# Kernel tuning notes

Hardware: AMD Instinct MI355X
Metric: run time of the kernel (lower is better)

Reference implementation:

```python
import jax, jax.numpy as jnp
import numpy as np

N = 150000
K = 64
C = 128


def setup_inputs() -> dict:
    key = jax.random.key(0)
    k1, k2, k3, k4 = jax.random.split(key, 4)
    H = 512
    W = 512
    pX = jax.random.randint(k1, (N,), 0, W, dtype=jnp.int32)
    pY = jax.random.randint(k2, (N,), 0, H, dtype=jnp.int32)
    vertMask = jax.random.normal(k3, (K, N), dtype=jnp.float32)
    feature = jax.random.normal(k4, (C, K), dtype=jnp.float32)
    return {"H": H, "W": W, "pX": pX, "pY": pY, "vertMask": vertMask, "feature": feature}


def reference(H, W, pX, pY, vertMask, feature):
    # [C, K] @ [K, N] -> [C, N]
    vals = jnp.matmul(feature, vertMask)
    out = jnp.zeros((feature.shape[0], H, W), dtype=feature.dtype)
    # scatter per-vertex features into the dense HxW canvas at irregular coords
    return out.at[:, pY, pX].set(vals)
```

## Files before the change

### kernel.cpp

```cpp
#include <hip/hip_runtime.h>

constexpr int KK = 64;
constexpr int CC = 128;

typedef float f32x4 __attribute__((ext_vector_type(4)));
typedef short short8 __attribute__((ext_vector_type(8)));
typedef unsigned short ushort_t;

__device__ inline ushort_t f2bf(float f) {
    union { float f; unsigned u; } v; v.f = f;
    unsigned r = v.u + 0x7FFFu + ((v.u >> 16) & 1u);
    return (ushort_t)(r >> 16);
}

__global__ __launch_bounds__(256) void prep_fused(
        const float* __restrict__ vm, ushort_t* __restrict__ vmT,
        const int* __restrict__ pX, const int* __restrict__ pY,
        const int* __restrict__ pW, int* __restrict__ winner,
        int N, int nTile) {
    int b = blockIdx.x;
    int t = threadIdx.x;
    if (b >= nTile) {
        int i = (b - nTile) * 256 + t;
        if (i < N) atomicMax(&winner[pY[i] * pW[0] + pX[i]], i + 1);
        return;
    }
    __shared__ float tile[KK][KK + 1];
    int n0 = b * KK;
    int lane = t & 63;
    int wv = t >> 6;
    int n = n0 + lane;
    #pragma unroll
    for (int r = 0; r < 16; ++r) {
        int k = r * 4 + wv;
        tile[k][lane] = (n < N) ? vm[(size_t)k * N + n] : 0.f;
    }
    __syncthreads();
    #pragma unroll
    for (int r = 0; r < 16; ++r) {
        int nl = r * 4 + wv;
        vmT[(size_t)(n0 + nl) * KK + lane] = f2bf(tile[lane][nl]);
    }
}

__global__ __launch_bounds__(256, 6) void produce_mfma(
        const int* __restrict__ winner, const ushort_t* __restrict__ vmT,
        const float* __restrict__ feature, float* __restrict__ out,
        int HW, int zrow) {
    int t = threadIdx.x;
    int p0 = blockIdx.x * 128;
    int wv = t >> 6;
    int L = t & 63;
    int lm = L & 15, q = L >> 4;
    int m0 = wv * 32;

    short8 afrag[2][2];
    #pragma unroll
    for (int mt = 0; mt < 2; ++mt)
        #pragma unroll
        for (int kh = 0; kh < 2; ++kh) {
            const float* fp = feature + (size_t)(m0 + mt * 16 + lm) * KK + kh * 32 + q * 8;
            f32x4 x0 = *(const f32x4*)fp;
            f32x4 x1 = *(const f32x4*)(fp + 4);
            short8 s;
            s[0] = (short)f2bf(x0[0]); s[1] = (short)f2bf(x0[1]);
            s[2] = (short)f2bf(x0[2]); s[3] = (short)f2bf(x0[3]);
            s[4] = (short)f2bf(x1[0]); s[5] = (short)f2bf(x1[1]);
            s[6] = (short)f2bf(x1[2]); s[7] = (short)f2bf(x1[3]);
            afrag[mt][kh] = s;
        }

    int wc[8];
    #pragma unroll
    for (int nt = 0; nt < 8; ++nt) {
        int w = winner[p0 + nt * 16 + lm];
        wc[nt] = (w > 0) ? (w - 1) : zrow;
    }

    #pragma unroll 4
    for (int nt = 0; nt < 8; ++nt) {
        const short8* row = (const short8*)(vmT + (size_t)wc[nt] * KK);
        short8 b0 = row[q];
        short8 b1 = row[4 + q];
        f32x4 acc0 = {0.f, 0.f, 0.f, 0.f};
        f32x4 acc1 = {0.f, 0.f, 0.f, 0.f};
        acc0 = __builtin_amdgcn_mfma_f32_16x16x32_bf16(afrag[0][0], b0, acc0, 0, 0, 0);
        acc0 = __builtin_amdgcn_mfma_f32_16x16x32_bf16(afrag[0][1], b1, acc0, 0, 0, 0);
        acc1 = __builtin_amdgcn_mfma_f32_16x16x32_bf16(afrag[1][0], b0, acc1, 0, 0, 0);
        acc1 = __builtin_amdgcn_mfma_f32_16x16x32_bf16(afrag[1][1], b1, acc1, 0, 0, 0);
        int pc = p0 + nt * 16 + lm;
        #pragma unroll
        for (int rr = 0; rr < 4; ++rr) {
            out[(size_t)(m0 + q * 4 + rr) * HW + pc] = acc0[rr];
            out[(size_t)(m0 + 16 + q * 4 + rr) * HW + pc] = acc1[rr];
        }
    }
}

extern "C" void kernel_launch(void* const* d_in, const int* in_sizes, int n_in,
                              void* d_out, int out_size, void* d_ws, size_t ws_size,
                              hipStream_t stream) {
    const int* dW = (const int*)d_in[1];
    const int* pX = (const int*)d_in[2];
    const int* pY = (const int*)d_in[3];
    const float* vm = (const float*)d_in[4];
    const float* feat = (const float*)d_in[5];
    float* out = (float*)d_out;

    int N = in_sizes[2];
    int HW = out_size / CC;

    int* winner = (int*)d_ws;
    size_t winBytes = (((size_t)HW * sizeof(int)) + 255) & ~(size_t)255;
    ushort_t* vmT = (ushort_t*)((char*)d_ws + winBytes);

    int nTile = (N + KK - 1) / KK;
    int nScat = (N + 255) / 256;

    hipLaunchKernelGGL(prep_fused, dim3(nTile + nScat), dim3(256), 0, stream,
                       vm, vmT, pX, pY, dW, winner, N, nTile);
    hipLaunchKernelGGL(produce_mfma, dim3(HW / 128), dim3(256), 0, stream,
                       winner, vmT, feat, out, HW, N);
}
```

Measured before the change: 195.1 us.

## Switch to 32x32 MFMA tiles and precompute bf16 features in prep kernel

The produce kernel now uses 32x32x16 bf16 MFMA instead of pairs of 16x16x32, so each wave covers 32 pixels per tile and writes 32 consecutive floats per output row, giving wider coalesced stores. The feature matrix is converted to bf16 once by an extra block in the prep kernel rather than by every produce block. The vmT transpose also switches to 16-byte vector stores. In exchange it uses larger accumulator registers per lane and adds one more block to the prep launch.

```diff
diff --git a/kernel.cpp b/kernel.cpp
--- a/kernel.cpp
+++ b/kernel.cpp
@@ -4,6 +4,7 @@
 constexpr int CC = 128;
 
 typedef float f32x4 __attribute__((ext_vector_type(4)));
+typedef float f32x16 __attribute__((ext_vector_type(16)));
 typedef short short8 __attribute__((ext_vector_type(8)));
 typedef unsigned short ushort_t;
 
@@ -15,14 +16,31 @@
 
 __global__ __launch_bounds__(256) void prep_fused(
         const float* __restrict__ vm, ushort_t* __restrict__ vmT,
+        const float* __restrict__ feat, ushort_t* __restrict__ featT,
         const int* __restrict__ pX, const int* __restrict__ pY,
         const int* __restrict__ pW, int* __restrict__ winner,
-        int N, int nTile) {
+        int N, int nTile, int nScat) {
     int b = blockIdx.x;
     int t = threadIdx.x;
     if (b >= nTile) {
-        int i = (b - nTile) * 256 + t;
-        if (i < N) atomicMax(&winner[pY[i] * pW[0] + pX[i]], i + 1);
+        if (b < nTile + nScat) {
+            int i = (b - nTile) * 256 + t;
+            if (i < N) atomicMax(&winner[pY[i] * pW[0] + pX[i]], i + 1);
+        } else {
+            int base = t * 32;
+            #pragma unroll
+            for (int j = 0; j < 4; ++j) {
+                const float* fp = feat + base + j * 8;
+                f32x4 x0 = *(const f32x4*)fp;
+                f32x4 x1 = *(const f32x4*)(fp + 4);
+                short8 s;
+                s[0] = (short)f2bf(x0[0]); s[1] = (short)f2bf(x0[1]);
+                s[2] = (short)f2bf(x0[2]); s[3] = (short)f2bf(x0[3]);
+                s[4] = (short)f2bf(x1[0]); s[5] = (short)f2bf(x1[1]);
+                s[6] = (short)f2bf(x1[2]); s[7] = (short)f2bf(x1[3]);
+                *(short8*)(featT + base + j * 8) = s;
+            }
+        }
         return;
     }
     __shared__ float tile[KK][KK + 1];
@@ -36,64 +54,60 @@
         tile[k][lane] = (n < N) ? vm[(size_t)k * N + n] : 0.f;
     }
     __syncthreads();
+    int c = lane & 7, r3 = lane >> 3;
     #pragma unroll
-    for (int r = 0; r < 16; ++r) {
-        int nl = r * 4 + wv;
-        vmT[(size_t)(n0 + nl) * KK + lane] = f2bf(tile[lane][nl]);
+    for (int s = 0; s < 2; ++s) {
+        int row = wv * 16 + s * 8 + r3;
+        short8 sv;
+        #pragma unroll
+        for (int j = 0; j < 8; ++j)
+            sv[j] = (short)f2bf(tile[c * 8 + j][row]);
+        *(short8*)(vmT + (size_t)(n0 + row) * KK + c * 8) = sv;
     }
 }
 
 __global__ __launch_bounds__(256, 6) void produce_mfma(
         const int* __restrict__ winner, const ushort_t* __restrict__ vmT,
-        const float* __restrict__ feature, float* __restrict__ out,
+        const ushort_t* __restrict__ featT, float* __restrict__ out,
         int HW, int zrow) {
     int t = threadIdx.x;
     int p0 = blockIdx.x * 128;
     int wv = t >> 6;
     int L = t & 63;
-    int lm = L & 15, q = L >> 4;
+    int cm = L & 31;
+    int h = L >> 5;
     int m0 = wv * 32;
 
-    short8 afrag[2][2];
+    short8 afrag[4];
     #pragma unroll
-    for (int mt = 0; mt < 2; ++mt)
-        #pragma unroll
-        for (int kh = 0; kh < 2; ++kh) {
-            const float* fp = feature + (size_t)(m0 + mt * 16 + lm) * KK + kh * 32 + q * 8;
-            f32x4 x0 = *(const f32x4*)fp;
-            f32x4 x1 = *(const f32x4*)(fp + 4);
-            short8 s;
-            s[0] = (short)f2bf(x0[0]); s[1] = (short)f2bf(x0[1]);
-            s[2] = (short)f2bf(x0[2]); s[3] = (short)f2bf(x0[3]);
-            s[4] = (short)f2bf(x1[0]); s[5] = (short)f2bf(x1[1]);
-            s[6] = (short)f2bf(x1[2]); s[7] = (short)f2bf(x1[3]);
-            afrag[mt][kh] = s;
-        }
+    for (int kk = 0; kk < 4; ++kk)
+        afrag[kk] = *(const short8*)(featT + (size_t)(m0 + cm) * KK + kk * 16 + h * 8);
 
-    int wc[8];
+    int wc[4];
     #pragma unroll
-    for (int nt = 0; nt < 8; ++nt) {
-        int w = winner[p0 + nt * 16 + lm];
+    for (int nt = 0; nt < 4; ++nt) {
+        int w = winner[p0 + nt * 32 + cm];
         wc[nt] = (w > 0) ? (w - 1) : zrow;
     }
 
-    #pragma unroll 4
-    for (int nt = 0; nt < 8; ++nt) {
+    #pragma unroll
+    for (int nt = 0; nt < 4; ++nt) {
         const short8* row = (const short8*)(vmT + (size_t)wc[nt] * KK);
-        short8 b0 = row[q];
-        short8 b1 = row[4 + q];
-        f32x4 acc0 = {0.f, 0.f, 0.f, 0.f};
-        f32x4 acc1 = {0.f, 0.f, 0.f, 0.f};
-        acc0 = __builtin_amdgcn_mfma_f32_16x16x32_bf16(afrag[0][0], b0, acc0, 0, 0, 0);
-        acc0 = __builtin_amdgcn_mfma_f32_16x16x32_bf16(afrag[0][1], b1, acc0, 0, 0, 0);
-        acc1 = __builtin_amdgcn_mfma_f32_16x16x32_bf16(afrag[1][0], b0, acc1, 0, 0, 0);
-        acc1 = __builtin_amdgcn_mfma_f32_16x16x32_bf16(afrag[1][1], b1, acc1, 0, 0, 0);
-        int pc = p0 + nt * 16 + lm;
+        short8 b0 = row[0 + h];
+        short8 b1 = row[2 + h];
+        short8 b2 = row[4 + h];
+        short8 b3 = row[6 + h];
+        f32x16 acc = {0.f, 0.f, 0.f, 0.f, 0.f, 0.f, 0.f, 0.f,
+                      0.f, 0.f, 0.f, 0.f, 0.f, 0.f, 0.f, 0.f};
+        acc = __builtin_amdgcn_mfma_f32_32x32x16_bf16(afrag[0], b0, acc, 0, 0, 0);
+        acc = __builtin_amdgcn_mfma_f32_32x32x16_bf16(afrag[1], b1, acc, 0, 0, 0);
+        acc = __builtin_amdgcn_mfma_f32_32x32x16_bf16(afrag[2], b2, acc, 0, 0, 0);
+        acc = __builtin_amdgcn_mfma_f32_32x32x16_bf16(afrag[3], b3, acc, 0, 0, 0);
+        int pc = p0 + nt * 32 + cm;
+        float* ob = out + (size_t)(m0 + 4 * h) * HW + pc;
         #pragma unroll
-        for (int rr = 0; rr < 4; ++rr) {
-            out[(size_t)(m0 + q * 4 + rr) * HW + pc] = acc0[rr];
-            out[(size_t)(m0 + 16 + q * 4 + rr) * HW + pc] = acc1[rr];
-        }
+        for (int r = 0; r < 16; ++r)
+            ob[(size_t)((r & 3) + 8 * (r >> 2)) * HW] = acc[r];
     }
 }
 
@@ -113,12 +127,13 @@
     int* winner = (int*)d_ws;
     size_t winBytes = (((size_t)HW * sizeof(int)) + 255) & ~(size_t)255;
     ushort_t* vmT = (ushort_t*)((char*)d_ws + winBytes);
+    ushort_t* featT = vmT + (size_t)((N + KK - 1) / KK) * KK * KK;
 
     int nTile = (N + KK - 1) / KK;
     int nScat = (N + 255) / 256;
 
-    hipLaunchKernelGGL(prep_fused, dim3(nTile + nScat), dim3(256), 0, stream,
-                       vm, vmT, pX, pY, dW, winner, N, nTile);
+    hipLaunchKernelGGL(prep_fused, dim3(nTile + nScat + 1), dim3(256), 0, stream,
+                       vm, vmT, feat, featT, pX, pY, dW, winner, N, nTile, nScat);
     hipLaunchKernelGGL(produce_mfma, dim3(HW / 128), dim3(256), 0, stream,
-                       winner, vmT, feat, out, HW, N);
+                       winner, vmT, featT, out, HW, N);
 }
```

Measured after the change: 189.9 us. 2.7% less time.
